# Performance work log

Measured on AMD Instinct MI355X. Metric: run time of the kernel, lower is better.

Reference implementation:

```python
import jax, jax.numpy as jnp
import numpy as np

B, H, W, C = 16, 64, 64, 512
WS, SS, NH = 8, 4, 16
HD = C // NH
N = WS * WS          # tokens per window = 64
NWH, NWW = H // WS, W // WS
NW = NWH * NWW       # windows per image = 64
HID = 2048
EPS = 1e-5

def _rel_pos_index():
    coords = np.stack(np.meshgrid(np.arange(WS), np.arange(WS), indexing='ij'))  # [2,ws,ws]
    cf = coords.reshape(2, -1)                      # [2,N]
    rel = cf[:, :, None] - cf[:, None, :]           # [2,N,N]
    rel = rel.transpose(1, 2, 0).astype(np.int64)   # [N,N,2]
    rel[:, :, 0] += WS - 1
    rel[:, :, 1] += WS - 1
    rel[:, :, 0] *= 2 * WS - 1
    return rel.sum(-1)                              # [N,N]

def _attn_mask():
    img = np.zeros((H, W), dtype=np.float32)
    cnt = 0
    sls = (slice(0, -WS), slice(-WS, -SS), slice(-SS, None))
    for hs in sls:
        for ws_ in sls:
            img[hs, ws_] = cnt
            cnt += 1
    mw = img.reshape(NWH, WS, NWW, WS).transpose(0, 2, 1, 3).reshape(-1, N)  # [nW,N]
    am = mw[:, None, :] - mw[:, :, None]            # [nW,N,N] (unsqueeze(1)-unsqueeze(2))
    return np.where(am != 0, np.float32(-100.0), np.float32(0.0))

_RPI = jnp.asarray(_rel_pos_index())
_AMASK = jnp.asarray(_attn_mask())

def _ln(x, g, b):
    m = jnp.mean(x, -1, keepdims=True)
    v = jnp.mean((x - m) ** 2, -1, keepdims=True)
    return (x - m) * jax.lax.rsqrt(v + EPS) * g + b

def setup_inputs() -> dict:
    key = jax.random.key(0)
    ks = jax.random.split(key, 8)
    s = 0.02
    return {
        'x': jax.random.normal(ks[0], (B, H * W, C), jnp.float32),
        'g1': jnp.ones((C,), jnp.float32), 'b1': jnp.zeros((C,), jnp.float32),
        'qkv_w': jax.random.normal(ks[1], (C, 3 * C), jnp.float32) * s,
        'qkv_b': jnp.zeros((3 * C,), jnp.float32),
        'proj_w': jax.random.normal(ks[2], (C, C), jnp.float32) * s,
        'proj_b': jnp.zeros((C,), jnp.float32),
        'rpb': jax.random.normal(ks[3], ((2 * WS - 1) ** 2, NH), jnp.float32) * s,
        'g2': jnp.ones((C,), jnp.float32), 'b2': jnp.zeros((C,), jnp.float32),
        'fc1_w': jax.random.normal(ks[4], (C, HID), jnp.float32) * s,
        'fc1_b': jnp.zeros((HID,), jnp.float32),
        'fc2_w': jax.random.normal(ks[5], (HID, C), jnp.float32) * s,
        'fc2_b': jnp.zeros((C,), jnp.float32),
    }

def reference(x, g1, b1, qkv_w, qkv_b, proj_w, proj_b, rpb, g2, b2, fc1_w, fc1_b, fc2_w, fc2_b):
    shortcut = x                                    # [B,L,C]
    xn = _ln(x, g1, b1).reshape(B, H, W, C)
    xs = jnp.roll(xn, (-SS, -SS), axis=(1, 2))      # cyclic shift
    # window partition -> [B*nW, N, C]
    xw = xs.reshape(B, NWH, WS, NWW, WS, C).transpose(0, 1, 3, 2, 4, 5).reshape(-1, N, C)
    # attention
    qkv = xw @ qkv_w + qkv_b                        # [Bw,N,3C]
    qkv = qkv.reshape(-1, N, 3, NH, HD).transpose(2, 0, 3, 1, 4)  # [3,Bw,NH,N,HD]
    q, k, v = qkv[0], qkv[1], qkv[2]
    scale = jnp.asarray(HD ** -0.5, xw.dtype)
    attn = jnp.einsum('bhnd,bhmd->bhnm', q, k) * scale            # [Bw,NH,N,N]
    bias = rpb[_RPI.reshape(-1)].reshape(N, N, NH).transpose(2, 0, 1)
    attn = attn + bias[None]
    attn = attn.reshape(B, NW, NH, N, N) + _AMASK[None, :, None]
    attn = jax.nn.softmax(attn.reshape(-1, NH, N, N), axis=-1)
    out = jnp.einsum('bhnm,bhmd->bhnd', attn, v)    # [Bw,NH,N,HD]
    out = out.transpose(0, 2, 1, 3).reshape(-1, N, C)
    out = out @ proj_w + proj_b
    # window reverse -> [B,H,W,C]
    xr = out.reshape(B, NWH, NWW, WS, WS, C).transpose(0, 1, 3, 2, 4, 5).reshape(B, H, W, C)
    xr = jnp.roll(xr, (SS, SS), axis=(1, 2)).reshape(B, H * W, C)
    x = shortcut + xr
    h = _ln(x, g2, b2)
    h = jax.nn.gelu(h @ fc1_w + fc1_b, approximate=False) @ fc2_w + fc2_b
    return x + h
```

## Files before the change

kernel.cpp:

```cpp
#include <hip/hip_runtime.h>
#include <hip/hip_bf16.h>

using f32x4  = __attribute__((ext_vector_type(4))) float;
using bf16x8 = __attribute__((ext_vector_type(8))) short;
using short8 = __attribute__((ext_vector_type(8))) short;
using s16x4  = __attribute__((ext_vector_type(4))) short;

#define DEVINL __device__ __forceinline__

DEVINL short f2bf(float f) {
  unsigned u = __builtin_bit_cast(unsigned, f);
  u += 0x7fffu + ((u >> 16) & 1u);
  return (short)(u >> 16);
}

DEVINL float gelu_fast(float v) {
  float t = __expf(-1.5957691216057308f * (v + 0.044715f * v * v * v));
  return v * __builtin_amdgcn_rcpf(1.0f + t);
}

#define GLDS16(g, l) __builtin_amdgcn_global_load_lds( \
    (const __attribute__((address_space(1))) void*)(g), \
    (__attribute__((address_space(3))) void*)(l), 16, 0, 0)

#define SBAR() __builtin_amdgcn_s_barrier()
#define WAITV(n) asm volatile("s_waitcnt vmcnt(" #n ")" ::: "memory")

__global__ __launch_bounds__(256)
void transpose_bf16(const float* __restrict__ in, short* __restrict__ out, int R, int C) {
  int idx = blockIdx.x * 256 + threadIdx.x;
  if (idx >= R * C) return;
  int c = idx / R, r = idx % R;
  out[idx] = f2bf(in[(size_t)r * C + c]);
}

__global__ __launch_bounds__(256)
void bias_expand(const float* __restrict__ rpb, float* __restrict__ BIASF) {
  int idx = blockIdx.x * 256 + threadIdx.x;
  int head = idx >> 12, n = (idx >> 6) & 63, m = idx & 63;
  int i1 = n >> 3, j1 = n & 7, i2 = m >> 3, j2 = m & 7;
  BIASF[idx] = rpb[((i1 - i2 + 7) * 15 + (j1 - j2 + 7)) * 16 + head];
}

template<int REMAP>
__global__ __launch_bounds__(256)
void ln_kernel(const float* __restrict__ X, const float* __restrict__ gamma,
               const float* __restrict__ beta, short* __restrict__ OUT) {
  const int lane = threadIdx.x & 63;
  const int wid  = threadIdx.x >> 6;
  const int t    = blockIdx.x * 4 + wid;
  const float* xp = X + (size_t)t * 512 + lane * 8;
  float4 a = *(const float4*)xp;
  float4 b = *(const float4*)(xp + 4);
  float s = a.x + a.y + a.z + a.w + b.x + b.y + b.z + b.w;
  float q = a.x*a.x + a.y*a.y + a.z*a.z + a.w*a.w
          + b.x*b.x + b.y*b.y + b.z*b.z + b.w*b.w;
#pragma unroll
  for (int d = 1; d < 64; d <<= 1) { s += __shfl_xor(s, d); q += __shfl_xor(q, d); }
  float mean = s * (1.0f / 512.0f);
  float var  = q * (1.0f / 512.0f) - mean * mean;
  float rstd = rsqrtf(var + 1e-5f);
  float4 g0 = *(const float4*)(gamma + lane * 8);
  float4 g1 = *(const float4*)(gamma + lane * 8 + 4);
  float4 b0 = *(const float4*)(beta + lane * 8);
  float4 b1 = *(const float4*)(beta + lane * 8 + 4);
  short8 o;
  o[0] = f2bf((a.x - mean) * rstd * g0.x + b0.x);
  o[1] = f2bf((a.y - mean) * rstd * g0.y + b0.y);
  o[2] = f2bf((a.z - mean) * rstd * g0.z + b0.z);
  o[3] = f2bf((a.w - mean) * rstd * g0.w + b0.w);
  o[4] = f2bf((b.x - mean) * rstd * g1.x + b1.x);
  o[5] = f2bf((b.y - mean) * rstd * g1.y + b1.y);
  o[6] = f2bf((b.z - mean) * rstd * g1.z + b1.z);
  o[7] = f2bf((b.w - mean) * rstd * g1.w + b1.w);
  size_t orow;
  if (REMAP) {
    int bb = t >> 12, l = t & 4095, hh = l >> 6, ww = l & 63;
    int hs = (hh + 60) & 63, ws2 = (ww + 60) & 63;
    orow = (size_t)(bb * 64 + (hs >> 3) * 8 + (ws2 >> 3)) * 64 + (hs & 7) * 8 + (ws2 & 7);
  } else {
    orow = (size_t)t;
  }
  *(short8*)(OUT + orow * 512 + lane * 8) = o;
}

__global__ __launch_bounds__(256)
void attn_core(const short* __restrict__ Q, const short* __restrict__ Kb,
               const short* __restrict__ VT, const float* __restrict__ BIASF,
               short* __restrict__ AOUT) {
  __shared__ short P[4][4096];
  const int tid = threadIdx.x, lane = tid & 63, wid = tid >> 6;
  const int lr = lane & 15, lg = lane >> 4;
  const int gw = blockIdx.x * 4 + wid;
  const int win = gw >> 4, head = gw & 15;
  const int wimg = win & 63, wh = wimg >> 3, ww = wimg & 7;
  const size_t qbase = (size_t)win * 64 * 512 + head * 32;
  short* Pb = P[wid];

  bf16x8 aq[4], bk[4];
#pragma unroll
  for (int tm = 0; tm < 4; ++tm) aq[tm] = *(const bf16x8*)(Q  + qbase + (size_t)(tm * 16 + lr) * 512 + lg * 8);
#pragma unroll
  for (int tn = 0; tn < 4; ++tn) bk[tn] = *(const bf16x8*)(Kb + qbase + (size_t)(tn * 16 + lr) * 512 + lg * 8);
  f32x4 sa[4][4] = {};
#pragma unroll
  for (int tm = 0; tm < 4; ++tm)
#pragma unroll
    for (int tn = 0; tn < 4; ++tn)
      sa[tm][tn] = __builtin_amdgcn_mfma_f32_16x16x32_bf16(aq[tm], bk[tn], sa[tm][tn], 0, 0, 0);

  const float* bias_h = BIASF + head * 4096;
  float inv[4][4];
#pragma unroll
  for (int tm = 0; tm < 4; ++tm) {
#pragma unroll
    for (int e = 0; e < 4; ++e) {
      const int n = tm * 16 + lg * 4 + e;
      const int i1 = n >> 3, j1 = n & 7;
      const int rh1 = (wh == 7) ? 1 + (i1 >> 2) : 0;
      const int rw1 = (ww == 7) ? 1 + (j1 >> 2) : 0;
      float v[4];
      float mx = -3.0e38f;
#pragma unroll
      for (int tn = 0; tn < 4; ++tn) {
        const int m = tn * 16 + lr;
        const int mi = (m >> 3), mj = m & 7;
        const int rh2 = (wh == 7) ? 1 + (mi >> 2) : 0;
        const int rw2 = (ww == 7) ? 1 + (mj >> 2) : 0;
        float val = sa[tm][tn][e] + bias_h[n * 64 + m]
                  + ((rh1 != rh2 || rw1 != rw2) ? -100.0f : 0.0f);
        v[tn] = val;
        mx = fmaxf(mx, val);
      }
#pragma unroll
      for (int d = 1; d < 16; d <<= 1) mx = fmaxf(mx, __shfl_xor(mx, d));
      float sum = 0.f;
#pragma unroll
      for (int tn = 0; tn < 4; ++tn) { v[tn] = __expf(v[tn] - mx); sum += v[tn]; }
#pragma unroll
      for (int d = 1; d < 16; d <<= 1) sum += __shfl_xor(sum, d);
      inv[tm][e] = 1.0f / sum;
      const int sw = (n & 7) << 3;
#pragma unroll
      for (int tn = 0; tn < 4; ++tn) Pb[n * 64 + ((tn * 16 + lr) ^ sw)] = f2bf(v[tn]);
    }
  }
  __syncthreads();

  f32x4 oa[4][2] = {};
  const short* vt = VT + (size_t)win * 32768 + head * 2048;
#pragma unroll
  for (int ks = 0; ks < 2; ++ks) {
    bf16x8 pa[4], bv[2];
#pragma unroll
    for (int tm = 0; tm < 4; ++tm) {
      const int r = tm * 16 + lr;
      pa[tm] = *(const bf16x8*)(Pb + r * 64 + ((ks * 32 + lg * 8) ^ ((r & 7) << 3)));
    }
#pragma unroll
    for (int t2 = 0; t2 < 2; ++t2) bv[t2] = *(const bf16x8*)(vt + (t2 * 16 + lr) * 64 + ks * 32 + lg * 8);
#pragma unroll
    for (int tm = 0; tm < 4; ++tm)
#pragma unroll
      for (int t2 = 0; t2 < 2; ++t2)
        oa[tm][t2] = __builtin_amdgcn_mfma_f32_16x16x32_bf16(pa[tm], bv[t2], oa[tm][t2], 0, 0, 0);
  }
#pragma unroll
  for (int tm = 0; tm < 4; ++tm)
#pragma unroll
    for (int t2 = 0; t2 < 2; ++t2)
#pragma unroll
      for (int e = 0; e < 4; ++e) {
        const int n = tm * 16 + lg * 4 + e;
        AOUT[((size_t)win * 64 + n) * 512 + head * 32 + t2 * 16 + lr] = f2bf(oa[tm][t2][e] * inv[tm][e]);
      }
}

template<int EPI, int K, int NX>
__global__ __launch_bounds__(256)
void gemm128v3(const short* __restrict__ Aa, const short* __restrict__ Bb,
               const float* __restrict__ bias, const float* __restrict__ resid,
               float* __restrict__ outf, short* __restrict__ outh) {
  constexpr int NT = K / 32;
  __shared__ short L[3][2][128 * 32];
  const int tid = threadIdx.x;
  const int lane = tid & 63, wid = tid >> 6;
  const int lr = lane & 15, lg = lane >> 4;
  const int wm = wid >> 1, wn = wid & 1;

  const int nwg = gridDim.x;
  const int id = blockIdx.x;
  const int id2 = (id & 7) * (nwg >> 3) + (id >> 3);
  const int mt    = (EPI == 1) ? (id2 % NX) : (id2 / NX);
  const int ntile = (EPI == 1) ? (id2 / NX) : (id2 % NX);
  const int m0 = mt * 128, n0 = ntile * 128;

  const int r0 = tid >> 2;
  const int cdb = (tid & 3) * 16;
  const int scol = ((tid & 3) * 8) ^ (((r0 >> 1) & 3) * 8);

  auto stage = [&](int slot, int kt) {
    char* s = (char*)L + slot * 16384;
    GLDS16(Aa + (size_t)(m0 + r0) * K + kt * 32 + scol,      s + r0 * 64 + cdb);
    GLDS16(Aa + (size_t)(m0 + r0 + 64) * K + kt * 32 + scol, s + (r0 + 64) * 64 + cdb);
    GLDS16(Bb + (size_t)(n0 + r0) * K + kt * 32 + scol,      s + 8192 + r0 * 64 + cdb);
    GLDS16(Bb + (size_t)(n0 + r0 + 64) * K + kt * 32 + scol, s + 8192 + (r0 + 64) * 64 + cdb);
  };

  const int xr = ((lr >> 1) & 3) * 16;
  const int acol = (lg * 16) ^ xr;

  f32x4 acc[4][4] = {};
  stage(0, 0);
  stage(1, 1);
  WAITV(4);
  SBAR();

  for (int t = 0; t < NT; ++t) {
    const char* Ls = (char*)L + (t % 3) * 16384;
    bf16x8 a[4], b[4];
#pragma unroll
    for (int i = 0; i < 4; ++i) a[i] = *(const bf16x8*)(Ls + (wm * 64 + i * 16 + lr) * 64 + acol);
#pragma unroll
    for (int j = 0; j < 4; ++j) b[j] = *(const bf16x8*)(Ls + 8192 + (wn * 64 + j * 16 + lr) * 64 + acol);
    if (t + 2 < NT) stage((t + 2) % 3, t + 2);
    __builtin_amdgcn_s_setprio(1);
#pragma unroll
    for (int i = 0; i < 4; ++i)
#pragma unroll
      for (int j = 0; j < 4; ++j)
        acc[i][j] = __builtin_amdgcn_mfma_f32_16x16x32_bf16(a[i], b[j], acc[i][j], 0, 0, 0);
    __builtin_amdgcn_s_setprio(0);
    if (t < NT - 2)       { WAITV(4); }
    else if (t == NT - 2) { WAITV(0); }
    SBAR();
  }

  if (EPI == 1) {
#pragma unroll
    for (int i = 0; i < 4; ++i) {
      const int h0 = m0 + wm * 64 + i * 16 + lg * 4;
      const float4 bi = *(const float4*)(bias + h0);
#pragma unroll
      for (int j = 0; j < 4; ++j) {
        const int tok = n0 + wn * 64 + j * 16 + lr;
        s16x4 o;
        o[0] = f2bf(gelu_fast(acc[i][j][0] + bi.x));
        o[1] = f2bf(gelu_fast(acc[i][j][1] + bi.y));
        o[2] = f2bf(gelu_fast(acc[i][j][2] + bi.z));
        o[3] = f2bf(gelu_fast(acc[i][j][3] + bi.w));
        *(s16x4*)(outh + (size_t)tok * 2048 + h0) = o;
      }
    }
  } else if (EPI == 0) {
#pragma unroll
    for (int j = 0; j < 4; ++j) {
      const int col = n0 + wn * 64 + j * 16 + lr;
      const float bc = bias[col];
#pragma unroll
      for (int i = 0; i < 4; ++i)
#pragma unroll
        for (int e = 0; e < 4; ++e) {
          const int row = m0 + wm * 64 + i * 16 + lg * 4 + e;
          float v = acc[i][j][e] + bc;
          const int wv = row >> 6, n = row & 63;
          const int bb = wv >> 6, wi = wv & 63;
          const int hs = (wi >> 3) * 8 + (n >> 3), ws2 = (wi & 7) * 8 + (n & 7);
          const int hh = (hs + 4) & 63, wwp = (ws2 + 4) & 63;
          const size_t orow = (size_t)bb * 4096 + hh * 64 + wwp;
          outf[orow * 512 + col] = resid[orow * 512 + col] + v;
        }
    }
  } else if (EPI == 2) {
#pragma unroll
    for (int j = 0; j < 4; ++j) {
      const int col = n0 + wn * 64 + j * 16 + lr;
      const float bc = bias[col];
#pragma unroll
      for (int i = 0; i < 4; ++i)
#pragma unroll
        for (int e = 0; e < 4; ++e) {
          const int row = m0 + wm * 64 + i * 16 + lg * 4 + e;
          outf[(size_t)row * 512 + col] = acc[i][j][e] + bc + resid[(size_t)row * 512 + col];
        }
    }
  } else {
    const int seg = n0 >> 9;
#pragma unroll
    for (int j = 0; j < 4; ++j) {
      const int col = n0 + wn * 64 + j * 16 + lr;
      const float bc = bias[col];
#pragma unroll
      for (int i = 0; i < 4; ++i) {
        const int row0 = m0 + wm * 64 + i * 16 + lg * 4;
        if (seg == 2) {
          const int cc = col - 1024;
          s16x4 o;
#pragma unroll
          for (int e = 0; e < 4; ++e) o[e] = f2bf(acc[i][j][e] + bc);
          *(s16x4*)(outh + 67108864 +
                    (size_t)((row0 >> 6) * 16 + (cc >> 5)) * 2048 + (cc & 31) * 64 + (row0 & 63)) = o;
        } else {
#pragma unroll
          for (int e = 0; e < 4; ++e) {
            const int row = row0 + e;
            float v = acc[i][j][e] + bc;
            if (seg == 0) outh[(size_t)row * 512 + col] = f2bf(v * 0.17677669529663687f);
            else          outh[33554432 + (size_t)row * 512 + (col - 512)] = f2bf(v);
          }
        }
      }
    }
  }
}

extern "C" void kernel_launch(void* const* d_in, const int* in_sizes, int n_in,
                              void* d_out, int out_size, void* d_ws, size_t ws_size,
                              hipStream_t stream) {
  (void)in_sizes; (void)n_in; (void)out_size; (void)ws_size;
  const float* x      = (const float*)d_in[0];
  const float* g1     = (const float*)d_in[1];
  const float* b1     = (const float*)d_in[2];
  const float* qkv_w  = (const float*)d_in[3];
  const float* qkv_b  = (const float*)d_in[4];
  const float* proj_w = (const float*)d_in[5];
  const float* proj_b = (const float*)d_in[6];
  const float* rpb    = (const float*)d_in[7];
  const float* g2     = (const float*)d_in[8];
  const float* b2     = (const float*)d_in[9];
  const float* fc1_w  = (const float*)d_in[10];
  const float* fc1_b  = (const float*)d_in[11];
  const float* fc2_w  = (const float*)d_in[12];
  const float* fc2_b  = (const float*)d_in[13];
  float* out = (float*)d_out;
  char* ws = (char*)d_ws;

  short* WQKVT  = (short*)(ws);
  short* WPROJT = (short*)(ws + 1572864);
  short* WFC1T  = (short*)(ws + 2097152);
  short* WFC2T  = (short*)(ws + 4194304);
  float* X2     = (float*)(ws + 6291456);
  float* BIASF  = (float*)(ws + 6291456);
  short* ATT    = (short*)(ws + 140509184);
  short* XW     = (short*)(ws + 207618048);
  short* QB     = (short*)(ws + 274726912);
  short* H1     = XW;
  short* X2N    = ATT;

  transpose_bf16<<<3072, 256, 0, stream>>>(qkv_w,  WQKVT, 512, 1536);
  transpose_bf16<<<1024, 256, 0, stream>>>(proj_w, WPROJT, 512, 512);
  transpose_bf16<<<4096, 256, 0, stream>>>(fc1_w,  WFC1T, 512, 2048);
  transpose_bf16<<<4096, 256, 0, stream>>>(fc2_w,  WFC2T, 2048, 512);
  bias_expand<<<256, 256, 0, stream>>>(rpb, BIASF);

  ln_kernel<1><<<16384, 256, 0, stream>>>(x, g1, b1, XW);
  gemm128v3<3, 512, 12><<<6144, 256, 0, stream>>>(XW, WQKVT, qkv_b, nullptr, nullptr, QB);
  attn_core<<<4096, 256, 0, stream>>>(QB, QB + 33554432, QB + 67108864, BIASF, ATT);
  gemm128v3<0, 512, 4><<<2048, 256, 0, stream>>>(ATT, WPROJT, proj_b, x, X2, nullptr);
  ln_kernel<0><<<16384, 256, 0, stream>>>(X2, g2, b2, X2N);
  gemm128v3<1, 512, 16><<<8192, 256, 0, stream>>>(WFC1T, X2N, fc1_b, nullptr, nullptr, H1);
  gemm128v3<2, 2048, 4><<<2048, 256, 0, stream>>>(H1, WFC2T, fc2_b, X2, out, nullptr);
}
```

Before: 869.5 us.

## Replace triple-buffered GEMM pipeline with single-buffer sync loop and two-wave occupancy

The GEMM kernel drops its three-stage LDS ring with explicit vmcnt waits, prefetch two tiles ahead and priority bumps. It now loads one K-tile into a single LDS buffer, syncs, computes and syncs again, and sets launch bounds to request two blocks per CU. The aim is to cut LDS footprint and register pressure so more workgroups are resident and hide latency through occupancy. The cost is that load/compute overlap inside each block is lost and every K step pays two full barriers.

```diff
diff --git a/kernel.cpp b/kernel.cpp
--- a/kernel.cpp
+++ b/kernel.cpp
@@ -22,9 +22,6 @@
 #define GLDS16(g, l) __builtin_amdgcn_global_load_lds( \
     (const __attribute__((address_space(1))) void*)(g), \
     (__attribute__((address_space(3))) void*)(l), 16, 0, 0)
-
-#define SBAR() __builtin_amdgcn_s_barrier()
-#define WAITV(n) asm volatile("s_waitcnt vmcnt(" #n ")" ::: "memory")
 
 __global__ __launch_bounds__(256)
 void transpose_bf16(const float* __restrict__ in, short* __restrict__ out, int R, int C) {
@@ -177,12 +174,11 @@
 }
 
 template<int EPI, int K, int NX>
-__global__ __launch_bounds__(256)
-void gemm128v3(const short* __restrict__ Aa, const short* __restrict__ Bb,
+__global__ __launch_bounds__(256, 2)
+void gemm128v5(const short* __restrict__ Aa, const short* __restrict__ Bb,
                const float* __restrict__ bias, const float* __restrict__ resid,
                float* __restrict__ outf, short* __restrict__ outh) {
-  constexpr int NT = K / 32;
-  __shared__ short L[3][2][128 * 32];
+  __shared__ short L[2][128 * 32];
   const int tid = threadIdx.x;
   const int lane = tid & 63, wid = tid >> 6;
   const int lr = lane & 15, lg = lane >> 4;
@@ -199,41 +195,26 @@
   const int cdb = (tid & 3) * 16;
   const int scol = ((tid & 3) * 8) ^ (((r0 >> 1) & 3) * 8);
 
-  auto stage = [&](int slot, int kt) {
-    char* s = (char*)L + slot * 16384;
-    GLDS16(Aa + (size_t)(m0 + r0) * K + kt * 32 + scol,      s + r0 * 64 + cdb);
-    GLDS16(Aa + (size_t)(m0 + r0 + 64) * K + kt * 32 + scol, s + (r0 + 64) * 64 + cdb);
-    GLDS16(Bb + (size_t)(n0 + r0) * K + kt * 32 + scol,      s + 8192 + r0 * 64 + cdb);
-    GLDS16(Bb + (size_t)(n0 + r0 + 64) * K + kt * 32 + scol, s + 8192 + (r0 + 64) * 64 + cdb);
-  };
-
-  const int xr = ((lr >> 1) & 3) * 16;
-  const int acol = (lg * 16) ^ xr;
+  const int acol = (lg * 16) ^ (((lr >> 1) & 3) * 16);
 
   f32x4 acc[4][4] = {};
-  stage(0, 0);
-  stage(1, 1);
-  WAITV(4);
-  SBAR();
-
-  for (int t = 0; t < NT; ++t) {
-    const char* Ls = (char*)L + (t % 3) * 16384;
+  for (int kt = 0; kt < K; kt += 32) {
+    GLDS16(Aa + (size_t)(m0 + r0) * K + kt + scol,      (char*)L + r0 * 64 + cdb);
+    GLDS16(Aa + (size_t)(m0 + r0 + 64) * K + kt + scol, (char*)L + (r0 + 64) * 64 + cdb);
+    GLDS16(Bb + (size_t)(n0 + r0) * K + kt + scol,      (char*)L + 8192 + r0 * 64 + cdb);
+    GLDS16(Bb + (size_t)(n0 + r0 + 64) * K + kt + scol, (char*)L + 8192 + (r0 + 64) * 64 + cdb);
+    __syncthreads();
     bf16x8 a[4], b[4];
 #pragma unroll
-    for (int i = 0; i < 4; ++i) a[i] = *(const bf16x8*)(Ls + (wm * 64 + i * 16 + lr) * 64 + acol);
-#pragma unroll
-    for (int j = 0; j < 4; ++j) b[j] = *(const bf16x8*)(Ls + 8192 + (wn * 64 + j * 16 + lr) * 64 + acol);
-    if (t + 2 < NT) stage((t + 2) % 3, t + 2);
-    __builtin_amdgcn_s_setprio(1);
+    for (int i = 0; i < 4; ++i) a[i] = *(const bf16x8*)((const char*)L + (wm * 64 + i * 16 + lr) * 64 + acol);
+#pragma unroll
+    for (int j = 0; j < 4; ++j) b[j] = *(const bf16x8*)((const char*)L + 8192 + (wn * 64 + j * 16 + lr) * 64 + acol);
 #pragma unroll
     for (int i = 0; i < 4; ++i)
 #pragma unroll
       for (int j = 0; j < 4; ++j)
         acc[i][j] = __builtin_amdgcn_mfma_f32_16x16x32_bf16(a[i], b[j], acc[i][j], 0, 0, 0);
-    __builtin_amdgcn_s_setprio(0);
-    if (t < NT - 2)       { WAITV(4); }
-    else if (t == NT - 2) { WAITV(0); }
-    SBAR();
+    __syncthreads();
   }
 
   if (EPI == 1) {
@@ -354,10 +335,10 @@
   bias_expand<<<256, 256, 0, stream>>>(rpb, BIASF);
 
   ln_kernel<1><<<16384, 256, 0, stream>>>(x, g1, b1, XW);
-  gemm128v3<3, 512, 12><<<6144, 256, 0, stream>>>(XW, WQKVT, qkv_b, nullptr, nullptr, QB);
+  gemm128v5<3, 512, 12><<<6144, 256, 0, stream>>>(XW, WQKVT, qkv_b, nullptr, nullptr, QB);
   attn_core<<<4096, 256, 0, stream>>>(QB, QB + 33554432, QB + 67108864, BIASF, ATT);
-  gemm128v3<0, 512, 4><<<2048, 256, 0, stream>>>(ATT, WPROJT, proj_b, x, X2, nullptr);
+  gemm128v5<0, 512, 4><<<2048, 256, 0, stream>>>(ATT, WPROJT, proj_b, x, X2, nullptr);
   ln_kernel<0><<<16384, 256, 0, stream>>>(X2, g2, b2, X2N);
-  gemm128v3<1, 512, 16><<<8192, 256, 0, stream>>>(WFC1T, X2N, fc1_b, nullptr, nullptr, H1);
-  gemm128v3<2, 2048, 4><<<2048, 256, 0, stream>>>(H1, WFC2T, fc2_b, X2, out, nullptr);
-}
+  gemm128v5<1, 512, 16><<<8192, 256, 0, stream>>>(WFC1T, X2N, fc1_b, nullptr, nullptr, H1);
+  gemm128v5<2, 2048, 4><<<2048, 256, 0, stream>>>(H1, WFC2T, fc2_b, X2, out, nullptr);
+}
```

Result: slower. 916.7 us (+5.4%).
